# Kernel optimization log

Measured on AMD Instinct MI355X. Metric: run time of the kernel, lower is better.

## Reference

```python
import jax, jax.numpy as jnp
import numpy as np

LEAK = 0.2   # LeakyReLU slope in CVAE
T = 0.07     # MoCo temperature
TOPK = 2
DISK = 15


def _mlp2(x, Wa, ba, Wb, bb):
    # Linear -> ReLU -> Linear -> ReLU (MoCo encoders)
    return jax.nn.relu(jax.nn.relu(x @ Wa + ba) @ Wb + bb)


def setup_inputs() -> dict:
    key = jax.random.key(0)
    ks = jax.random.split(key, 32)
    B, R, V, F, L = 16384, 512, 1000, 300, 512

    def gn(k, shape, scale=0.05):
        return jax.random.normal(k, shape, dtype=jnp.float32) * scale

    inp = {}
    inp["logits"] = jax.random.normal(ks[0], (B, R), dtype=jnp.float32)
    inp["rels"] = jax.random.randint(ks[1], (R, 2), 0, V, dtype=jnp.int64)
    inp["rel_dict"] = jax.random.normal(ks[2], (V, F), dtype=jnp.float32)
    inp["eps1"] = jax.random.normal(ks[3], (B, L), dtype=jnp.float32)  # eps in ae.forward
    inp["eps2"] = jax.random.normal(ks[4], (B, L), dtype=jnp.float32)  # eps for z_
    # CVAE params (feature_size=300, class_size=300, latent_size=512)
    inp["W1"] = gn(ks[5], (F + F, 512)); inp["b1"] = jnp.zeros((512,), jnp.float32)
    inp["Wmu"] = gn(ks[6], (512, L));   inp["bmu"] = jnp.zeros((L,), jnp.float32)
    inp["Wls"] = gn(ks[7], (512, L));   inp["bls"] = jnp.zeros((L,), jnp.float32)
    inp["W3"] = gn(ks[8], (L + F, 512)); inp["b3"] = jnp.zeros((512,), jnp.float32)
    inp["W4"] = gn(ks[9], (512, F));    inp["b4"] = jnp.zeros((F,), jnp.float32)
    # MoCo encoder_inp (== encoder_k, since momentum update of identical params is a no-op)
    inp["iW1"] = gn(ks[10], (F, 512)); inp["ib1"] = jnp.zeros((512,), jnp.float32)
    inp["iW2"] = gn(ks[11], (512, 512)); inp["ib2"] = jnp.zeros((512,), jnp.float32)
    # MoCo encoder_z
    inp["zW1"] = gn(ks[12], (512, 512)); inp["zb1"] = jnp.zeros((512,), jnp.float32)
    inp["zW2"] = gn(ks[13], (512, 512)); inp["zb2"] = jnp.zeros((512,), jnp.float32)
    return inp


def reference(logits, rels, rel_dict, eps1, eps2,
              W1, b1, Wmu, bmu, Wls, bls, W3, b3, W4, b4,
              iW1, ib1, iW2, ib2, zW1, zb1, zW2, zb2):
    B = logits.shape[0]
    # sort descending / ascending over relation classes
    idx_desc = jnp.argsort(-logits, axis=1)
    idx_asc = jnp.argsort(logits, axis=1)
    top = idx_desc[:, :TOPK]        # [B,2]
    dis = idx_asc[:, :DISK]         # [B,15]

    keys = rels[:, 1]               # [R] indices into rel_dict
    # gathered features are all .detach()-ed in the original code
    pos1 = jax.lax.stop_gradient(rel_dict[keys[top[:, 0]]])   # [B,300]
    pos2 = jax.lax.stop_gradient(rel_dict[keys[top[:, 1]]])   # [B,300]
    neg = jax.lax.stop_gradient(rel_dict[keys[dis]])          # [B,15,300]

    # ---- CVAE forward (batched over B instead of the python loop) ----
    h1 = jax.nn.leaky_relu(jnp.concatenate([pos1, pos2], axis=1) @ W1 + b1, LEAK)
    mu = h1 @ Wmu + bmu              # [B,512]
    log_std = h1 @ Wls + bls         # [B,512]
    std = jnp.exp(log_std)
    z = mu + eps1 * std              # reparametrize inside ae.forward
    h3 = jax.nn.leaky_relu(jnp.concatenate([z, pos2], axis=1) @ W3 + b3, LEAK)
    recon = jnp.tanh(h3 @ W4 + b4)   # [B,300]

    recon_loss = jnp.sum((recon - pos1) ** 2)
    kl_loss = jnp.sum(-0.5 * (1.0 + 2.0 * log_std - mu ** 2 - jnp.exp(2.0 * log_std)))
    loss_vae = (recon_loss + kl_loss).reshape(1)

    z_ = mu + eps2 * std             # second, independent reparametrize for MoCo

    # ---- MoCo forward (batched) ----
    z_p = _mlp2(z_, zW1, zb1, zW2, zb2)                       # [B,512]
    pos_vec = _mlp2(pos1, iW1, ib1, iW2, ib2)                 # [B,512]
    # encoder_k params equal encoder_inp params (copied at init, momentum no-op); no grad
    neg_p = jax.lax.stop_gradient(_mlp2(neg, iW1, ib1, iW2, ib2))  # [B,15,512]

    pos = jnp.sum(z_p * pos_vec, axis=-1, keepdims=True)      # [B,1]
    negl = jnp.einsum('bd,bnd->bn', z_p, neg_p)               # [B,15]
    lg = jnp.concatenate([pos, negl], axis=1) / T             # [B,16]
    # cross entropy with label 0, mean over batch-of-1 then summed over the loop
    loss_csl = jnp.sum(-jax.nn.log_softmax(lg, axis=-1)[:, 0]).reshape(1)

    z_rel = jnp.concatenate([jnp.zeros((1, 512), z_p.dtype), z_p], axis=0)  # [B+1,512]
    return (loss_vae, loss_csl, z_rel)
```

## Files before the change

### kernel.cpp

```cpp
#include <hip/hip_runtime.h>
#include <math.h>

#define B_ 16384
#define R_ 512
#define V_ 1000
#define F_ 300
#define FP_ 320
#define L_ 512
#define H_ 512
#define LEAK_ 0.2f
#define TEMP_ 0.07f
#define DISK_ 15

#define NCSL_BLK (B_ / 4)
#define NKL_BLK  1024
#define NREC_BLK (3 * 128)

typedef short short8 __attribute__((ext_vector_type(8)));
typedef float float4v __attribute__((ext_vector_type(4)));

__device__ __forceinline__ float waveReduceSum(float v) {
#pragma unroll
    for (int off = 32; off; off >>= 1) v += __shfl_xor(v, off);
    return v;
}

__device__ __forceinline__ short f2bf(float f) {
    unsigned u = __float_as_uint(f);
    unsigned r = (u + 0x7FFFu + ((u >> 16) & 1u)) >> 16;
    return (short)r;
}

__device__ __forceinline__ void gld16(const short* g, short* l) {
    __builtin_amdgcn_global_load_lds(
        (const __attribute__((address_space(1))) void*)g,
        (__attribute__((address_space(3))) void*)l, 16, 0, 0);
}

__device__ __forceinline__ void xcd_swizzle(int& bx, int& by) {
    int gx = gridDim.x;
    int nwg = gx * gridDim.y;
    int wg = blockIdx.x + gx * blockIdx.y;
    int cpx = nwg >> 3;
    int swz = (wg & 7) * cpx + (wg >> 3);
    bx = swz % gx;
    by = swz / gx;
}

__device__ __forceinline__ int xcd_swizzle_flat() {
    int nwg = gridDim.x;
    int wg = blockIdx.x;
    int cpx = nwg >> 3;
    return (wg & 7) * cpx + (wg >> 3);
}

__global__ __launch_bounds__(64) void topk_kernel(
    const float* __restrict__ logits, int* __restrict__ top0,
    int* __restrict__ top1, int* __restrict__ dis) {
    int b = blockIdx.x;
    int lane = threadIdx.x;
    const float* lp = logits + (size_t)b * R_;
    float4 va = *(const float4*)&lp[lane * 8];
    float4 vb = *(const float4*)&lp[lane * 8 + 4];
    float v[8] = {va.x, va.y, va.z, va.w, vb.x, vb.y, vb.z, vb.w};
    unsigned u[8];
#pragma unroll
    for (int i = 0; i < 8; ++i) {
        int f = __float_as_int(v[i]);
        u[i] = (unsigned)f ^ ((unsigned)(f >> 31) | 0x80000000u);
    }
    unsigned long long t1 = 0ull, t2 = 0ull;
#pragma unroll
    for (int i = 0; i < 8; ++i) {
        unsigned long long k =
            ((unsigned long long)u[i] << 9) | (unsigned)(511 - (lane * 8 + i));
        if (k > t1) { t2 = t1; t1 = k; }
        else if (k > t2) t2 = k;
    }
#pragma unroll
    for (int off = 32; off; off >>= 1) {
        unsigned long long o1 = __shfl_xor(t1, off);
        unsigned long long o2 = __shfl_xor(t2, off);
        unsigned long long hi = t1 > o1 ? t1 : o1;
        unsigned long long lo = t1 > o1 ? o1 : t1;
        unsigned long long m2 = t2 > o2 ? t2 : o2;
        t1 = hi;
        t2 = lo > m2 ? lo : m2;
    }
    int i0 = 511 - (int)(t1 & 511u);
    int i1 = 511 - (int)(t2 & 511u);

    unsigned k32[8];
#pragma unroll
    for (int i = 0; i < 8; ++i) {
        int idx = lane * 8 + i;
        k32[i] = (u[i] & 0xFFFFFE00u) | (unsigned)idx;
        if (idx == i0 || idx == i1) k32[i] = 0xFFFFFFFFu;
    }
    unsigned lmin = k32[0];
#pragma unroll
    for (int i = 1; i < 8; ++i) lmin = min(lmin, k32[i]);
    int dloc[DISK_];
#pragma unroll
    for (int t = 0; t < DISK_; ++t) {
        unsigned w = lmin;
#pragma unroll
        for (int off = 32; off; off >>= 1) w = min(w, __shfl_xor(w, off));
        int idx = (int)(w & 0x1FFu);
        dloc[t] = idx;
        if ((idx >> 3) == lane) {
            k32[idx & 7] = 0xFFFFFFFFu;
            lmin = k32[0];
#pragma unroll
            for (int i = 1; i < 8; ++i) lmin = min(lmin, k32[i]);
        }
    }
    if (lane == 0) {
        top0[b] = i0; top1[b] = i1;
#pragma unroll
        for (int t = 0; t < DISK_; ++t) dis[b * DISK_ + t] = dloc[t];
    }
}

__global__ __launch_bounds__(FP_) void gather_d(
    const int* __restrict__ rels32, const float* __restrict__ rel_dict,
    float* __restrict__ d_table, short* __restrict__ dt) {
    __shared__ int s_i64;
    int tid = threadIdx.x, r = blockIdx.x;
    if (tid == 0) s_i64 = 1;
    __syncthreads();
    if (rels32[2 * tid + 1] != 0) s_i64 = 0;
    __syncthreads();
    int key = s_i64 ? rels32[4 * r + 2] : rels32[2 * r + 1];
    if (tid < F_) {
        float v = rel_dict[(size_t)key * F_ + tid];
        d_table[(size_t)r * F_ + tid] = v;
        dt[(size_t)r * FP_ + tid] = f2bf(v);
    } else {
        dt[(size_t)r * FP_ + tid] = 0;
    }
}

#define NT_ 11
struct TransArgs {
    const float* W[NT_];
    short* Wt[NT_];
    int row_off[NT_];
    int K[NT_];
    int Kpad[NT_];
    int N[NT_];
    int Npad[NT_];
    int ilv[NT_];
};
__global__ __launch_bounds__(256) void transpose_all(TransArgs ta) {
    int z = blockIdx.z;
    const float* W = ta.W[z];
    short* Wt = ta.Wt[z];
    int row_off = ta.row_off[z];
    int K = ta.K[z], Kpad = ta.Kpad[z], N = ta.N[z], Npad = ta.Npad[z];
    int ilv = ta.ilv[z];
    int k0 = blockIdx.x * 32, n0 = blockIdx.y * 32;
    if (k0 >= Kpad || n0 >= Npad) return;
    __shared__ float tile[32][33];
    int tx = threadIdx.x & 31, ty = threadIdx.x >> 5;
#pragma unroll
    for (int i = 0; i < 4; ++i) {
        int k = k0 + i * 8 + ty, n = n0 + tx;
        tile[i * 8 + ty][tx] = (k < K && n < N) ? W[(size_t)(row_off + k) * N + n] : 0.f;
    }
    __syncthreads();
#pragma unroll
    for (int i = 0; i < 4; ++i) {
        int n = n0 + i * 8 + ty, k = k0 + tx;
        if (n < Npad && k < Kpad) {
            int orow = (ilv >= 0) ? (ilv + 128 * (n >> 6) + (n & 63)) : n;
            Wt[(size_t)orow * Kpad + k] = f2bf(tile[tx][i * 8 + ty]);
        }
    }
}

__global__ __launch_bounds__(256) void h1_kernel(
    const float* __restrict__ Pcat, const float* __restrict__ b1,
    const int* __restrict__ top0, const int* __restrict__ top1,
    short* __restrict__ h1b) {
    int idx = blockIdx.x * 256 + threadIdx.x;
    int b = idx >> 9, j = idx & 511;
    float v = Pcat[(size_t)top0[b] * 2048 + j] + Pcat[(size_t)top1[b] * 2048 + 512 + j] + b1[j];
    h1b[idx] = f2bf(v > 0.f ? v : LEAK_ * v);
}

__global__ __launch_bounds__(256) void ipre_kernel(
    const float* __restrict__ Pcat, const float* __restrict__ ib1,
    short* __restrict__ ipre) {
    int idx = blockIdx.x * 256 + threadIdx.x;
    int r = idx >> 9, j = idx & 511;
    float v = Pcat[(size_t)r * 2048 + 1536 + j] + ib1[j];
    ipre[idx] = f2bf(v > 0.f ? v : 0.f);
}

__device__ __forceinline__ void gemm_core(
    const short* __restrict__ A, const short* __restrict__ Wt,
    int row0, int col0, int tid, short* As, short* Bs,
    float4v (&acc)[2][8]) {
    const int K = 512;
    int lane = tid & 63, wv = tid >> 6;
    int lm = lane & 15, q = lane >> 4;
    int ga0 = row0 + wv * 16 + (lane >> 2);
    int gb0 = col0 + wv * 16 + (lane >> 2);
    int koff = (lane & 3) * 8;
    short* lA0 = As + (wv * 16) * 32;
    short* lA1 = As + (64 + wv * 16) * 32;
    short* lB0 = Bs + (wv * 16) * 32;
    short* lB1 = Bs + (64 + wv * 16) * 32;
#pragma unroll
    for (int i = 0; i < 2; ++i)
#pragma unroll
        for (int j = 0; j < 8; ++j) acc[i][j] = {0.f, 0.f, 0.f, 0.f};
    for (int k0 = 0; k0 < K; k0 += 32) {
        __syncthreads();
        gld16(&A[(size_t)ga0 * K + k0 + koff], lA0);
        gld16(&A[(size_t)(ga0 + 64) * K + k0 + koff], lA1);
        gld16(&Wt[(size_t)gb0 * K + k0 + koff], lB0);
        gld16(&Wt[(size_t)(gb0 + 64) * K + k0 + koff], lB1);
        __syncthreads();
        short8 af[2], bf[8];
#pragma unroll
        for (int mt = 0; mt < 2; ++mt)
            af[mt] = *(const short8*)&As[(wv * 32 + mt * 16 + lm) * 32 + q * 8];
#pragma unroll
        for (int nt = 0; nt < 8; ++nt)
            bf[nt] = *(const short8*)&Bs[(nt * 16 + lm) * 32 + q * 8];
#pragma unroll
        for (int mt = 0; mt < 2; ++mt)
#pragma unroll
            for (int nt = 0; nt < 8; ++nt)
                acc[mt][nt] = __builtin_amdgcn_mfma_f32_16x16x32_bf16(
                    af[mt], bf[nt], acc[mt][nt], 0, 0, 0);
    }
}

template <int MODE>
__device__ __forceinline__ void epi_std(
    float4v (&acc)[2][8], int row0, int col0, int tid, void* C,
    const float* __restrict__ bias, const float* __restrict__ table,
    int tld, const int* __restrict__ rowsel) {
    int lane = tid & 63, wv = tid >> 6;
    int lm = lane & 15, q = lane >> 4;
#pragma unroll
    for (int mt = 0; mt < 2; ++mt)
#pragma unroll
        for (int r = 0; r < 4; ++r) {
            int grow = row0 + wv * 32 + mt * 16 + q * 4 + r;
            int trow = (MODE == 1) ? rowsel[grow] : 0;
#pragma unroll
            for (int nt = 0; nt < 8; ++nt) {
                int gcol = col0 + nt * 16 + lm;
                float v = acc[mt][nt][r] + bias[gcol];
                if (MODE == 1) {
                    v += table[(size_t)trow * tld + gcol];
                    v = v > 0.f ? v : LEAK_ * v;
                } else {
                    v = v > 0.f ? v : 0.f;
                }
                if (MODE == 4)
                    ((float*)C)[(size_t)grow * 512 + gcol] = v;
                else
                    ((short*)C)[(size_t)grow * 512 + gcol] = f2bf(v);
            }
        }
}

__device__ __forceinline__ void epi_recon(
    float4v (&acc)[2][8], int row0, int col0, int tid,
    const float* __restrict__ b4, const float* __restrict__ d_table,
    const int* __restrict__ top0, float* __restrict__ p_rec, int pidx,
    float* sred) {
    int lane = tid & 63, wv = tid >> 6;
    int lm = lane & 15, q = lane >> 4;
    float lsum = 0.f;
#pragma unroll
    for (int mt = 0; mt < 2; ++mt)
#pragma unroll
        for (int r = 0; r < 4; ++r) {
            int grow = row0 + wv * 32 + mt * 16 + q * 4 + r;
            int trow = top0[grow];
#pragma unroll
            for (int nt = 0; nt < 8; ++nt) {
                int gcol = col0 + nt * 16 + lm;
                if (gcol < F_) {
                    float v = tanhf(acc[mt][nt][r] + b4[gcol]);
                    float d = v - d_table[(size_t)trow * F_ + gcol];
                    lsum += d * d;
                }
            }
        }
    lsum = waveReduceSum(lsum);
    if (lane == 0) sred[wv] = lsum;
    __syncthreads();
    if (tid == 0) p_rec[pidx] = sred[0] + sred[1] + sred[2] + sred[3];
}

__global__ __launch_bounds__(256) void gemm_muls(
    const short* __restrict__ A, const short* __restrict__ Wt,
    short* __restrict__ Cz, short* __restrict__ Cz2,
    const float* __restrict__ bmu, const float* __restrict__ bls,
    const float* __restrict__ eps1, const float* __restrict__ eps2,
    float* __restrict__ p_kl) {
    __shared__ __align__(16) short As[128 * 32];
    __shared__ __align__(16) short Bs[128 * 32];
    __shared__ float sred[4];
    int tid = threadIdx.x;
    int bx, by;
    xcd_swizzle(bx, by);
    int row0 = by * 128, col0 = bx * 128;
    float4v acc[2][8];
    gemm_core(A, Wt, row0, col0, tid, As, Bs, acc);

    int lane = tid & 63, wv = tid >> 6;
    int lm = lane & 15, q = lane >> 4;
    float kl = 0.f;
#pragma unroll
    for (int mt = 0; mt < 2; ++mt) {
#pragma unroll
        for (int r = 0; r < 4; ++r) {
            int grow = row0 + wv * 32 + mt * 16 + q * 4 + r;
#pragma unroll
            for (int jj = 0; jj < 4; ++jj) {
                int j = (col0 >> 1) + jj * 16 + lm;
                float m = acc[mt][jj][r] + bmu[j];
                float lsv = acc[mt][jj + 4][r] + bls[j];
                float s = __expf(lsv);
                size_t ix = (size_t)grow * 512 + j;
                Cz[ix]  = f2bf(m + eps1[ix] * s);
                Cz2[ix] = f2bf(m + eps2[ix] * s);
                kl += -0.5f * (1.f + 2.f * lsv - m * m - s * s);
            }
        }
    }
    kl = waveReduceSum(kl);
    if (lane == 0) sred[wv] = kl;
    __syncthreads();
    if (tid == 0)
        p_kl[bx + gridDim.x * by] = sred[0] + sred[1] + sred[2] + sred[3];
}

__global__ __launch_bounds__(256) void dual12_kernel(
    const short* __restrict__ zA, const short* __restrict__ Wt3,
    short* __restrict__ h3out, const float* __restrict__ b3,
    const float* __restrict__ Ptab, const int* __restrict__ top1,
    const short* __restrict__ zpA, const short* __restrict__ Wtz1,
    short* __restrict__ tout, const float* __restrict__ zb1,
    const short* __restrict__ ipreA, const short* __restrict__ Wti2,
    float* __restrict__ ipostC, const float* __restrict__ ib2,
    int jobSel) {
    __shared__ __align__(16) short As[128 * 32];
    __shared__ __align__(16) short Bs[128 * 32];
    int tid = threadIdx.x;
    int wg = xcd_swizzle_flat();
    int job;
    if (jobSel >= 0) {
        job = jobSel;
    } else {
        job = (wg < 512) ? 0 : (wg < 1024 ? 1 : 2);
        wg -= (job == 1) ? 512 : (job == 2 ? 1024 : 0);
    }
    int bx = wg & 3, by = wg >> 2;
    int row0 = by * 128, col0 = bx * 128;
    float4v acc[2][8];
    if (job == 0) {
        gemm_core(zA, Wt3, row0, col0, tid, As, Bs, acc);
        epi_std<1>(acc, row0, col0, tid, h3out, b3, Ptab, 2048, top1);
    } else if (job == 1) {
        gemm_core(zpA, Wtz1, row0, col0, tid, As, Bs, acc);
        epi_std<2>(acc, row0, col0, tid, tout, zb1, nullptr, 0, nullptr);
    } else {
        gemm_core(ipreA, Wti2, row0, col0, tid, As, Bs, acc);
        epi_std<4>(acc, row0, col0, tid, ipostC, ib2, nullptr, 0, nullptr);
    }
}

__global__ __launch_bounds__(256) void dual34_kernel(
    const short* __restrict__ tA, const short* __restrict__ Wtz2,
    float* __restrict__ zpout, const float* __restrict__ zb2,
    const short* __restrict__ h3A, const short* __restrict__ Wt4,
    const float* __restrict__ b4, const float* __restrict__ d_table,
    const int* __restrict__ top0, float* __restrict__ p_rec, int jobSel) {
    __shared__ __align__(16) short As[128 * 32];
    __shared__ __align__(16) short Bs[128 * 32];
    __shared__ float sred[4];
    int tid = threadIdx.x;
    int wg = xcd_swizzle_flat();
    int job;
    if (jobSel >= 0) {
        job = jobSel;
    } else {
        job = (wg < 512) ? 0 : 1;
        if (job == 1) wg -= 512;
    }
    float4v acc[2][8];
    if (job == 0) {
        int bx = wg & 3, by = wg >> 2;
        int row0 = by * 128, col0 = bx * 128;
        gemm_core(tA, Wtz2, row0, col0, tid, As, Bs, acc);
        epi_std<4>(acc, row0, col0, tid, zpout, zb2, nullptr, 0, nullptr);
    } else {
        int bx = wg % 3, by = wg / 3;
        int row0 = by * 128, col0 = bx * 128;
        gemm_core(h3A, Wt4, row0, col0, tid, As, Bs, acc);
        epi_recon(acc, row0, col0, tid, b4, d_table, top0, p_rec,
                  bx + 3 * by, sred);
    }
}

template <int EPI, int KK>
__global__ __launch_bounds__(256) void gemm_mfma(
    const short* __restrict__ A, const short* __restrict__ Wt,
    void* __restrict__ C, int ldc, const float* __restrict__ bias,
    const float* __restrict__ table, int tld,
    const int* __restrict__ rowsel, float* __restrict__ lossp, int N) {
    __shared__ __align__(16) short Asl[2][128][40];
    __shared__ __align__(16) short Bsl[2][64][40];
    int tid = threadIdx.x;
    int lane = tid & 63, wv = tid >> 6;
    int lm = lane & 15, q = lane >> 4;
    int bx, by;
    xcd_swizzle(bx, by);
    int row0 = by * 128;
    int col0 = bx * 64;

    float4v acc[2][4];
#pragma unroll
    for (int i = 0; i < 2; ++i)
#pragma unroll
        for (int j = 0; j < 4; ++j) acc[i][j] = {0.f, 0.f, 0.f, 0.f};

    uint4 aReg[2], bReg;
    int ar0 = tid >> 2, ak = (tid & 3) * 8;
    int ar1 = (tid + 256) >> 2;
    int br = tid >> 2, bk = (tid & 3) * 8;

    auto loadG = [&](int k0) {
        aReg[0] = *(const uint4*)&A[(size_t)(row0 + ar0) * KK + k0 + ak];
        aReg[1] = *(const uint4*)&A[(size_t)(row0 + ar1) * KK + k0 + ak];
        bReg    = *(const uint4*)&Wt[(size_t)(col0 + br) * KK + k0 + bk];
    };
    auto storeL = [&](int p) {
        *(uint4*)&Asl[p][ar0][ak] = aReg[0];
        *(uint4*)&Asl[p][ar1][ak] = aReg[1];
        *(uint4*)&Bsl[p][br][bk]  = bReg;
    };

    int p = 0;
    loadG(0);
    storeL(0);
    for (int k0 = 0; k0 < KK; k0 += 32) {
        __syncthreads();
        bool more = (k0 + 32) < KK;
        if (more) loadG(k0 + 32);
        short8 af[2], bfr[4];
#pragma unroll
        for (int mt = 0; mt < 2; ++mt)
            af[mt] = *(const short8*)&Asl[p][wv * 32 + mt * 16 + lm][q * 8];
#pragma unroll
        for (int nt = 0; nt < 4; ++nt)
            bfr[nt] = *(const short8*)&Bsl[p][nt * 16 + lm][q * 8];
#pragma unroll
        for (int mt = 0; mt < 2; ++mt)
#pragma unroll
            for (int nt = 0; nt < 4; ++nt)
                acc[mt][nt] = __builtin_amdgcn_mfma_f32_16x16x32_bf16(
                    af[mt], bfr[nt], acc[mt][nt], 0, 0, 0);
        if (more) { p ^= 1; storeL(p); }
    }

#pragma unroll
    for (int mt = 0; mt < 2; ++mt) {
#pragma unroll
        for (int r = 0; r < 4; ++r) {
            int grow = row0 + wv * 32 + mt * 16 + q * 4 + r;
#pragma unroll
            for (int nt = 0; nt < 4; ++nt) {
                int gcol = col0 + nt * 16 + lm;
                float v = acc[mt][nt][r];
                if (EPI == 4) { v += bias[gcol]; v = v > 0.f ? v : 0.f; }
                ((float*)C)[(size_t)grow * ldc + gcol] = v;
            }
        }
    }
}

__global__ __launch_bounds__(256) void csl_kernel(
    const float* __restrict__ zp, const float* __restrict__ ipost,
    const int* __restrict__ top0, const int* __restrict__ dis,
    float* __restrict__ partial_csl) {
    __shared__ float sred[4];
    int w = threadIdx.x >> 6, lane = threadIdx.x & 63;
    int b = blockIdx.x * 4 + w;
    const float* zr = zp + (size_t)b * 512;
    float z[8];
#pragma unroll
    for (int i = 0; i < 8; ++i) z[i] = zr[i * 64 + lane];
    int cand[16];
    cand[0] = top0[b];
#pragma unroll
    for (int n = 0; n < DISK_; ++n) cand[n + 1] = dis[b * DISK_ + n];
    float s[16];
#pragma unroll
    for (int c = 0; c < 16; ++c) {
        const float* ip = ipost + (size_t)cand[c] * 512;
        float a = 0.f;
#pragma unroll
        for (int i = 0; i < 8; ++i) a += z[i] * ip[i * 64 + lane];
        s[c] = a;
    }
#pragma unroll
    for (int off = 32; off; off >>= 1) {
        float o[16];
#pragma unroll
        for (int c = 0; c < 16; ++c) o[c] = __shfl_xor(s[c], off);
#pragma unroll
        for (int c = 0; c < 16; ++c) s[c] += o[c];
    }
    if (lane == 0) {
        float m = s[0];
#pragma unroll
        for (int c = 1; c < 16; ++c) m = fmaxf(m, s[c]);
        float se = 0.f;
#pragma unroll
        for (int c = 0; c < 16; ++c) se += __expf((s[c] - m) / TEMP_);
        sred[w] = -((s[0] - m) / TEMP_ - __logf(se));
    }
    __syncthreads();
    if (threadIdx.x == 0)
        partial_csl[blockIdx.x] = sred[0] + sred[1] + sred[2] + sred[3];
}

__global__ __launch_bounds__(256) void finalize_kernel(
    const float* __restrict__ pkl, const float* __restrict__ prec,
    const float* __restrict__ pcsl, float* __restrict__ out) {
    __shared__ float red[4][2];
    int tid = threadIdx.x;
    out[2 + tid] = 0.f;
    out[2 + 256 + tid] = 0.f;
    float a0 = 0.f, a1 = 0.f;
    for (int i = tid; i < NKL_BLK; i += 256) a0 += pkl[i];
    for (int i = tid; i < NREC_BLK; i += 256) a0 += prec[i];
    for (int i = tid; i < NCSL_BLK; i += 256) a1 += pcsl[i];
    a0 = waveReduceSum(a0);
    a1 = waveReduceSum(a1);
    int lane = tid & 63, w = tid >> 6;
    if (lane == 0) { red[w][0] = a0; red[w][1] = a1; }
    __syncthreads();
    if (tid == 0) out[0] = red[0][0] + red[1][0] + red[2][0] + red[3][0];
    if (tid == 1) out[1] = red[0][1] + red[1][1] + red[2][1] + red[3][1];
}

extern "C" void kernel_launch(void* const* d_in, const int* in_sizes, int n_in,
                              void* d_out, int out_size, void* d_ws, size_t ws_size,
                              hipStream_t stream) {
    const float* logits  = (const float*)d_in[0];
    const int*   rels    = (const int*)d_in[1];
    const float* rel_dict= (const float*)d_in[2];
    const float* eps1    = (const float*)d_in[3];
    const float* eps2    = (const float*)d_in[4];
    const float* W1  = (const float*)d_in[5];
    const float* b1  = (const float*)d_in[6];
    const float* Wmu = (const float*)d_in[7];
    const float* bmu = (const float*)d_in[8];
    const float* Wls = (const float*)d_in[9];
    const float* bls = (const float*)d_in[10];
    const float* W3  = (const float*)d_in[11];
    const float* b3  = (const float*)d_in[12];
    const float* W4  = (const float*)d_in[13];
    const float* b4  = (const float*)d_in[14];
    const float* iW1 = (const float*)d_in[15];
    const float* ib1 = (const float*)d_in[16];
    const float* iW2 = (const float*)d_in[17];
    const float* ib2 = (const float*)d_in[18];
    const float* zW1 = (const float*)d_in[19];
    const float* zb1 = (const float*)d_in[20];
    const float* zW2 = (const float*)d_in[21];
    const float* zb2 = (const float*)d_in[22];
    float* out = (float*)d_out;

    char* wsp = (char*)d_ws;
    size_t off = 0;
    auto alloc = [&](size_t bytes) { void* p = wsp + off; off += (bytes + 255) & ~(size_t)255; return p; };
    int*   top0    = (int*)alloc(B_ * 4);
    int*   top1    = (int*)alloc(B_ * 4);
    int*   dis     = (int*)alloc(B_ * DISK_ * 4);
    float* d_table = (float*)alloc((size_t)R_ * F_ * 4);
    short* dt      = (short*)alloc((size_t)R_ * FP_ * 2);
    short* Wcat_t  = (short*)alloc((size_t)2048 * FP_ * 2);
    float* Pcat    = (float*)alloc((size_t)R_ * 2048 * 4);
    short* ipre    = (short*)alloc((size_t)R_ * H_ * 2);
    float* ipost   = (float*)alloc((size_t)R_ * H_ * 4);
    short* Wt_muls = (short*)alloc((size_t)1024 * 512 * 2);
    short* Wt_3    = (short*)alloc((size_t)512 * 512 * 2);
    short* Wt_z1   = (short*)alloc((size_t)512 * 512 * 2);
    short* Wt_z2   = (short*)alloc((size_t)512 * 512 * 2);
    short* Wt_4    = (short*)alloc((size_t)384 * 512 * 2);
    short* Wt_i2   = (short*)alloc((size_t)512 * 512 * 2);
    short* bfA     = (short*)alloc((size_t)B_ * H_ * 2);
    short* bfB     = (short*)alloc((size_t)B_ * H_ * 2);
    short* bfC     = (short*)alloc((size_t)B_ * H_ * 2);
    float* p_csl   = (float*)alloc(NCSL_BLK * 4);
    float* p_kl    = (float*)alloc(NKL_BLK * 4);
    float* p_rec   = (float*)alloc(NREC_BLK * 4);
    size_t bfD_bytes = (size_t)B_ * H_ * 2;
    bool merged = (off + bfD_bytes + 256) <= ws_size;
    short* bfD = merged ? (short*)alloc(bfD_bytes) : bfB;

    topk_kernel<<<B_, 64, 0, stream>>>(logits, top0, top1, dis);
    gather_d<<<R_, FP_, 0, stream>>>(rels, rel_dict, d_table, dt);

    TransArgs ta;
    auto set = [&](int i, const float* W, short* Wt, int ro, int K, int Kp, int N, int Np, int ilv) {
        ta.W[i] = W; ta.Wt[i] = Wt; ta.row_off[i] = ro; ta.K[i] = K;
        ta.Kpad[i] = Kp; ta.N[i] = N; ta.Npad[i] = Np; ta.ilv[i] = ilv;
    };
    set(0, Wmu, Wt_muls, 0, 512, 512, 512, 512, 0);
    set(1, Wls, Wt_muls, 0, 512, 512, 512, 512, 64);
    set(2, W3,  Wt_3,  0, 512, 512, 512, 512, -1);
    set(3, zW1, Wt_z1, 0, 512, 512, 512, 512, -1);
    set(4, zW2, Wt_z2, 0, 512, 512, 512, 512, -1);
    set(5, W4,  Wt_4,  0, 512, 512, 300, 384, -1);
    set(6, W1,  Wcat_t,              0,  F_, FP_, 512, 512, -1);
    set(7, W1,  Wcat_t + 512 * FP_,  F_, F_, FP_, 512, 512, -1);
    set(8, W3,  Wcat_t + 1024 * FP_, L_, F_, FP_, 512, 512, -1);
    set(9, iW1, Wcat_t + 1536 * FP_, 0,  F_, FP_, 512, 512, -1);
    set(10, iW2, Wt_i2, 0, 512, 512, 512, 512, -1);
    transpose_all<<<dim3(16, 16, NT_), 256, 0, stream>>>(ta);

    gemm_mfma<5, FP_><<<dim3(32, 4), 256, 0, stream>>>(
        dt, Wcat_t, Pcat, 2048, nullptr, nullptr, 0, nullptr, nullptr, 2048);
    ipre_kernel<<<R_ * H_ / 256, 256, 0, stream>>>(Pcat, ib1, ipre);
    h1_kernel<<<B_ * H_ / 256, 256, 0, stream>>>(Pcat, b1, top0, top1, bfA);

    gemm_muls<<<dim3(8, 128), 256, 0, stream>>>(
        bfA, Wt_muls, bfB, bfC, bmu, bls, eps1, eps2, p_kl);

    if (merged) {
        dual12_kernel<<<1040, 256, 0, stream>>>(
            bfB, Wt_3, bfA, b3, Pcat + 1024, top1,
            bfC, Wt_z1, bfD, zb1,
            ipre, Wt_i2, ipost, ib2, -1);
        dual34_kernel<<<896, 256, 0, stream>>>(
            bfD, Wt_z2, out + 2 + L_, zb2,
            bfA, Wt_4, b4, d_table, top0, p_rec, -1);
    } else {
        dual12_kernel<<<512, 256, 0, stream>>>(
            bfB, Wt_3, bfA, b3, Pcat + 1024, top1,
            bfC, Wt_z1, bfD, zb1, ipre, Wt_i2, ipost, ib2, 0);
        dual12_kernel<<<512, 256, 0, stream>>>(
            bfB, Wt_3, bfA, b3, Pcat + 1024, top1,
            bfC, Wt_z1, bfD, zb1, ipre, Wt_i2, ipost, ib2, 1);
        dual12_kernel<<<16, 256, 0, stream>>>(
            bfB, Wt_3, bfA, b3, Pcat + 1024, top1,
            bfC, Wt_z1, bfD, zb1, ipre, Wt_i2, ipost, ib2, 2);
        dual34_kernel<<<512, 256, 0, stream>>>(
            bfD, Wt_z2, out + 2 + L_, zb2,
            bfA, Wt_4, b4, d_table, top0, p_rec, 0);
        dual34_kernel<<<384, 256, 0, stream>>>(
            bfD, Wt_z2, out + 2 + L_, zb2,
            bfA, Wt_4, b4, d_table, top0, p_rec, 1);
    }

    csl_kernel<<<NCSL_BLK, 256, 0, stream>>>(out + 2 + L_, ipost, top0, dis, p_csl);
    finalize_kernel<<<1, 256, 0, stream>>>(p_kl, p_rec, p_csl, out);
}
```

Before: 388.9 us.

## Load GEMM fragments directly from global memory with register double-buffering, drop LDS

The shared GEMM core used by several fused kernels no longer stages A and W tiles through LDS with global_load_lds and two barriers per k-step. Each lane now loads its MFMA fragments straight from global memory into registers, with a two-stage ping-pong prefetch. This removes the barriers and the LDS traffic. In exchange, the four waves each fetch the same B tile separately, rows are read with 16-byte strided accesses that coalesce poorly, and the extra fragment registers may lower occupancy.

```diff
diff --git a/kernel.cpp b/kernel.cpp
--- a/kernel.cpp
+++ b/kernel.cpp
@@ -29,12 +29,6 @@
     unsigned u = __float_as_uint(f);
     unsigned r = (u + 0x7FFFu + ((u >> 16) & 1u)) >> 16;
     return (short)r;
-}
-
-__device__ __forceinline__ void gld16(const short* g, short* l) {
-    __builtin_amdgcn_global_load_lds(
-        (const __attribute__((address_space(1))) void*)g,
-        (__attribute__((address_space(3))) void*)l, 16, 0, 0);
 }
 
 __device__ __forceinline__ void xcd_swizzle(int& bx, int& by) {
@@ -198,44 +192,49 @@
     ipre[idx] = f2bf(v > 0.f ? v : 0.f);
 }
 
+__device__ __forceinline__ void load_frags(
+    const short* __restrict__ aBase, const short* __restrict__ bBase,
+    int k0, short8 (&af)[2], short8 (&bf)[8]) {
+#pragma unroll
+    for (int mt = 0; mt < 2; ++mt)
+        af[mt] = *(const short8*)&aBase[(size_t)mt * 16 * 512 + k0];
+#pragma unroll
+    for (int nt = 0; nt < 8; ++nt)
+        bf[nt] = *(const short8*)&bBase[(size_t)nt * 16 * 512 + k0];
+}
+
 __device__ __forceinline__ void gemm_core(
     const short* __restrict__ A, const short* __restrict__ Wt,
-    int row0, int col0, int tid, short* As, short* Bs,
-    float4v (&acc)[2][8]) {
-    const int K = 512;
+    int row0, int col0, int tid, float4v (&acc)[2][8]) {
     int lane = tid & 63, wv = tid >> 6;
     int lm = lane & 15, q = lane >> 4;
-    int ga0 = row0 + wv * 16 + (lane >> 2);
-    int gb0 = col0 + wv * 16 + (lane >> 2);
-    int koff = (lane & 3) * 8;
-    short* lA0 = As + (wv * 16) * 32;
-    short* lA1 = As + (64 + wv * 16) * 32;
-    short* lB0 = Bs + (wv * 16) * 32;
-    short* lB1 = Bs + (64 + wv * 16) * 32;
+    const short* aBase = A + (size_t)(row0 + wv * 32 + lm) * 512 + q * 8;
+    const short* bBase = Wt + (size_t)(col0 + lm) * 512 + q * 8;
 #pragma unroll
     for (int i = 0; i < 2; ++i)
 #pragma unroll
         for (int j = 0; j < 8; ++j) acc[i][j] = {0.f, 0.f, 0.f, 0.f};
-    for (int k0 = 0; k0 < K; k0 += 32) {
-        __syncthreads();
-        gld16(&A[(size_t)ga0 * K + k0 + koff], lA0);
-        gld16(&A[(size_t)(ga0 + 64) * K + k0 + koff], lA1);
-        gld16(&Wt[(size_t)gb0 * K + k0 + koff], lB0);
-        gld16(&Wt[(size_t)(gb0 + 64) * K + k0 + koff], lB1);
-        __syncthreads();
-        short8 af[2], bf[8];
-#pragma unroll
-        for (int mt = 0; mt < 2; ++mt)
-            af[mt] = *(const short8*)&As[(wv * 32 + mt * 16 + lm) * 32 + q * 8];
-#pragma unroll
-        for (int nt = 0; nt < 8; ++nt)
-            bf[nt] = *(const short8*)&Bs[(nt * 16 + lm) * 32 + q * 8];
+
+    short8 aP[2], bP[8], aQ[2], bQ[8];
+    load_frags(aBase, bBase, 0, aP, bP);
+#pragma unroll
+    for (int it = 0; it < 16; it += 2) {
+        if (it + 1 < 16) load_frags(aBase, bBase, (it + 1) * 32, aQ, bQ);
 #pragma unroll
         for (int mt = 0; mt < 2; ++mt)
 #pragma unroll
             for (int nt = 0; nt < 8; ++nt)
                 acc[mt][nt] = __builtin_amdgcn_mfma_f32_16x16x32_bf16(
-                    af[mt], bf[nt], acc[mt][nt], 0, 0, 0);
+                    aP[mt], bP[nt], acc[mt][nt], 0, 0, 0);
+        if (it + 2 < 16) load_frags(aBase, bBase, (it + 2) * 32, aP, bP);
+        if (it + 1 < 16) {
+#pragma unroll
+            for (int mt = 0; mt < 2; ++mt)
+#pragma unroll
+                for (int nt = 0; nt < 8; ++nt)
+                    acc[mt][nt] = __builtin_amdgcn_mfma_f32_16x16x32_bf16(
+                        aQ[mt], bQ[nt], acc[mt][nt], 0, 0, 0);
+        }
     }
 }
 
@@ -306,15 +305,13 @@
     const float* __restrict__ bmu, const float* __restrict__ bls,
     const float* __restrict__ eps1, const float* __restrict__ eps2,
     float* __restrict__ p_kl) {
-    __shared__ __align__(16) short As[128 * 32];
-    __shared__ __align__(16) short Bs[128 * 32];
     __shared__ float sred[4];
     int tid = threadIdx.x;
     int bx, by;
     xcd_swizzle(bx, by);
     int row0 = by * 128, col0 = bx * 128;
     float4v acc[2][8];
-    gemm_core(A, Wt, row0, col0, tid, As, Bs, acc);
+    gemm_core(A, Wt, row0, col0, tid, acc);
 
     int lane = tid & 63, wv = tid >> 6;
     int lm = lane & 15, q = lane >> 4;
@@ -353,8 +350,6 @@
     const short* __restrict__ ipreA, const short* __restrict__ Wti2,
     float* __restrict__ ipostC, const float* __restrict__ ib2,
     int jobSel) {
-    __shared__ __align__(16) short As[128 * 32];
-    __shared__ __align__(16) short Bs[128 * 32];
     int tid = threadIdx.x;
     int wg = xcd_swizzle_flat();
     int job;
@@ -368,13 +363,13 @@
     int row0 = by * 128, col0 = bx * 128;
     float4v acc[2][8];
     if (job == 0) {
-        gemm_core(zA, Wt3, row0, col0, tid, As, Bs, acc);
+        gemm_core(zA, Wt3, row0, col0, tid, acc);
         epi_std<1>(acc, row0, col0, tid, h3out, b3, Ptab, 2048, top1);
     } else if (job == 1) {
-        gemm_core(zpA, Wtz1, row0, col0, tid, As, Bs, acc);
+        gemm_core(zpA, Wtz1, row0, col0, tid, acc);
         epi_std<2>(acc, row0, col0, tid, tout, zb1, nullptr, 0, nullptr);
     } else {
-        gemm_core(ipreA, Wti2, row0, col0, tid, As, Bs, acc);
+        gemm_core(ipreA, Wti2, row0, col0, tid, acc);
         epi_std<4>(acc, row0, col0, tid, ipostC, ib2, nullptr, 0, nullptr);
     }
 }
@@ -385,8 +380,6 @@
     const short* __restrict__ h3A, const short* __restrict__ Wt4,
     const float* __restrict__ b4, const float* __restrict__ d_table,
     const int* __restrict__ top0, float* __restrict__ p_rec, int jobSel) {
-    __shared__ __align__(16) short As[128 * 32];
-    __shared__ __align__(16) short Bs[128 * 32];
     __shared__ float sred[4];
     int tid = threadIdx.x;
     int wg = xcd_swizzle_flat();
@@ -401,12 +394,12 @@
     if (job == 0) {
         int bx = wg & 3, by = wg >> 2;
         int row0 = by * 128, col0 = bx * 128;
-        gemm_core(tA, Wtz2, row0, col0, tid, As, Bs, acc);
+        gemm_core(tA, Wtz2, row0, col0, tid, acc);
         epi_std<4>(acc, row0, col0, tid, zpout, zb2, nullptr, 0, nullptr);
     } else {
         int bx = wg % 3, by = wg / 3;
         int row0 = by * 128, col0 = bx * 128;
-        gemm_core(h3A, Wt4, row0, col0, tid, As, Bs, acc);
+        gemm_core(h3A, Wt4, row0, col0, tid, acc);
         epi_recon(acc, row0, col0, tid, b4, d_table, top0, p_rec,
                   bx + 3 * by, sred);
     }
```

After: 566.8 us. 45.7% more time.

## Double GEMM K-tile to 64 and XOR-swizzle LDS layout to avoid bank conflicts

Applied to the files above, without the earlier changes.

The shared GEMM core now stages a K-slice of 64 per iteration instead of 32, which halves the number of barrier pairs and global-to-LDS load rounds per tile. The LDS layout becomes 64-element rows with an XOR swizzle of 16-byte chunks by row index, so fragment reads across lanes land in different banks. Each iteration runs two MFMA sub-steps over the staged data. LDS use per block doubles, which can lower occupancy.

```diff
diff --git a/kernel.cpp b/kernel.cpp
--- a/kernel.cpp
+++ b/kernel.cpp
@@ -198,6 +198,10 @@
     ipre[idx] = f2bf(v > 0.f ? v : 0.f);
 }
 
+__device__ __forceinline__ const short8* frag_at(const short* buf, int row, int cb) {
+    return (const short8*)&buf[row * 64 + ((cb ^ (row & 7)) * 8)];
+}
+
 __device__ __forceinline__ void gemm_core(
     const short* __restrict__ A, const short* __restrict__ Wt,
     int row0, int col0, int tid, short* As, short* Bs,
@@ -205,37 +209,41 @@
     const int K = 512;
     int lane = tid & 63, wv = tid >> 6;
     int lm = lane & 15, q = lane >> 4;
-    int ga0 = row0 + wv * 16 + (lane >> 2);
-    int gb0 = col0 + wv * 16 + (lane >> 2);
-    int koff = (lane & 3) * 8;
-    short* lA0 = As + (wv * 16) * 32;
-    short* lA1 = As + (64 + wv * 16) * 32;
-    short* lB0 = Bs + (wv * 16) * 32;
-    short* lB1 = Bs + (64 + wv * 16) * 32;
+    int rsub = lane >> 3;
+    int kswz = ((lane & 7) ^ rsub) * 8;
+    int ga = row0 + wv * 8 + rsub;
+    int gb = col0 + wv * 8 + rsub;
+    short* lA = As + (wv * 8) * 64;
+    short* lB = Bs + (wv * 8) * 64;
 #pragma unroll
     for (int i = 0; i < 2; ++i)
 #pragma unroll
         for (int j = 0; j < 8; ++j) acc[i][j] = {0.f, 0.f, 0.f, 0.f};
-    for (int k0 = 0; k0 < K; k0 += 32) {
+
+    for (int k0 = 0; k0 < K; k0 += 64) {
         __syncthreads();
-        gld16(&A[(size_t)ga0 * K + k0 + koff], lA0);
-        gld16(&A[(size_t)(ga0 + 64) * K + k0 + koff], lA1);
-        gld16(&Wt[(size_t)gb0 * K + k0 + koff], lB0);
-        gld16(&Wt[(size_t)(gb0 + 64) * K + k0 + koff], lB1);
+#pragma unroll
+        for (int j = 0; j < 4; ++j) {
+            gld16(&A[(size_t)(ga + 32 * j) * K + k0 + kswz], lA + 32 * j * 64);
+            gld16(&Wt[(size_t)(gb + 32 * j) * K + k0 + kswz], lB + 32 * j * 64);
+        }
         __syncthreads();
-        short8 af[2], bf[8];
-#pragma unroll
-        for (int mt = 0; mt < 2; ++mt)
-            af[mt] = *(const short8*)&As[(wv * 32 + mt * 16 + lm) * 32 + q * 8];
-#pragma unroll
-        for (int nt = 0; nt < 8; ++nt)
-            bf[nt] = *(const short8*)&Bs[(nt * 16 + lm) * 32 + q * 8];
-#pragma unroll
-        for (int mt = 0; mt < 2; ++mt)
+#pragma unroll
+        for (int kk = 0; kk < 2; ++kk) {
+            short8 af[2], bf[8];
+#pragma unroll
+            for (int mt = 0; mt < 2; ++mt)
+                af[mt] = *frag_at(As, wv * 32 + mt * 16 + lm, kk * 4 + q);
 #pragma unroll
             for (int nt = 0; nt < 8; ++nt)
-                acc[mt][nt] = __builtin_amdgcn_mfma_f32_16x16x32_bf16(
-                    af[mt], bf[nt], acc[mt][nt], 0, 0, 0);
+                bf[nt] = *frag_at(Bs, nt * 16 + lm, kk * 4 + q);
+#pragma unroll
+            for (int mt = 0; mt < 2; ++mt)
+#pragma unroll
+                for (int nt = 0; nt < 8; ++nt)
+                    acc[mt][nt] = __builtin_amdgcn_mfma_f32_16x16x32_bf16(
+                        af[mt], bf[nt], acc[mt][nt], 0, 0, 0);
+        }
     }
 }
 
@@ -306,8 +314,8 @@
     const float* __restrict__ bmu, const float* __restrict__ bls,
     const float* __restrict__ eps1, const float* __restrict__ eps2,
     float* __restrict__ p_kl) {
-    __shared__ __align__(16) short As[128 * 32];
-    __shared__ __align__(16) short Bs[128 * 32];
+    __shared__ __align__(16) short As[128 * 64];
+    __shared__ __align__(16) short Bs[128 * 64];
     __shared__ float sred[4];
     int tid = threadIdx.x;
     int bx, by;
@@ -353,8 +361,8 @@
     const short* __restrict__ ipreA, const short* __restrict__ Wti2,
     float* __restrict__ ipostC, const float* __restrict__ ib2,
     int jobSel) {
-    __shared__ __align__(16) short As[128 * 32];
-    __shared__ __align__(16) short Bs[128 * 32];
+    __shared__ __align__(16) short As[128 * 64];
+    __shared__ __align__(16) short Bs[128 * 64];
     int tid = threadIdx.x;
     int wg = xcd_swizzle_flat();
     int job;
@@ -385,8 +393,8 @@
     const short* __restrict__ h3A, const short* __restrict__ Wt4,
     const float* __restrict__ b4, const float* __restrict__ d_table,
     const int* __restrict__ top0, float* __restrict__ p_rec, int jobSel) {
-    __shared__ __align__(16) short As[128 * 32];
-    __shared__ __align__(16) short Bs[128 * 32];
+    __shared__ __align__(16) short As[128 * 64];
+    __shared__ __align__(16) short Bs[128 * 64];
     __shared__ float sred[4];
     int tid = threadIdx.x;
     int wg = xcd_swizzle_flat();
```

After: 380.2 us. 2.2% less time.
